# Kernel tuning notes

Hardware: AMD Instinct MI355X
Metric: run time of the kernel (lower is better)

Reference implementation:

```python
import jax, jax.numpy as jnp
import numpy as np

H = 32; L = 4; HEADS = 8; VC = 16; BIG = 1e9

def _unit(v):
    return v * jax.lax.rsqrt(jnp.sum(v * v, -1, keepdims=True) + 1e-8)

def _dihedrals(bb):
    n = bb.shape[0]
    X = bb[:, :3].reshape(n * 3, 3)
    U = _unit(X[1:] - X[:-1])
    u2, u1, u0 = U[:-2], U[1:-1], U[2:]
    n2 = _unit(jnp.cross(u2, u1)); n1 = _unit(jnp.cross(u1, u0))
    cosD = jnp.clip(jnp.sum(n2 * n1, -1), -1 + 1e-6, 1 - 1e-6)
    D = jnp.sign(jnp.sum(u2 * n1, -1)) * jnp.arccos(cosD)
    D = jnp.pad(D, (1, 2)).reshape(n, 3)
    return jnp.concatenate([jnp.cos(D), jnp.sin(D)], -1)

def _orientations(x):
    f = jnp.pad(_unit(x[1:] - x[:-1]), ((0, 1), (0, 0)))
    b = jnp.pad(_unit(x[:-1] - x[1:]), ((1, 0), (0, 0)))
    return jnp.stack([f, b], -2)

def _virtual_cb(bb):
    n_, ca, c = bb[:, 0], bb[:, 1], bb[:, 2]
    b = ca - n_; cc = c - ca; a = jnp.cross(b, cc)
    return -0.58273431 * a + 0.56802827 * b - 0.54067466 * cc + ca

def _rbf(d, nbin=16, dmax=20.0):
    mu = jnp.linspace(0.0, dmax, nbin); sig = dmax / nbin
    return jnp.exp(-(((d[..., None] - mu) / sig) ** 2))

def _pos_emb(didx, nemb=16):
    freq = jnp.exp(jnp.arange(0, nemb, 2, dtype=jnp.float32) * (-np.log(10000.0) / nemb))
    ang = didx[..., None].astype(jnp.float32) * freq
    return jnp.concatenate([jnp.cos(ang), jnp.sin(ang)], -1)

def _edge_rot(vec):
    # per-edge rotation aligning edge direction to e_y (equiformer-style)
    nrm = _unit(vec)
    helper = jnp.where(jnp.abs(nrm[..., 2:3]) > 0.99, jnp.array([1.0, 0.0, 0.0]), jnp.array([0.0, 0.0, 1.0]))
    z = _unit(jnp.cross(nrm, helper))
    x = jnp.cross(nrm, z)
    return jnp.stack([x, nrm, z], axis=-2)

def _rot(R, x):
    return jnp.concatenate([x[..., :1, :], jnp.einsum('...ij,...jc->...ic', R, x[..., 1:, :])], -2)

def _rot_inv(R, x):
    return jnp.concatenate([x[..., :1, :], jnp.einsum('...ji,...jc->...ic', R, x[..., 1:, :])], -2)

def _norm_so3(x, g0, b0, g1):
    x0 = x[..., 0, :]; x1 = x[..., 1:, :]
    mu = jnp.mean(x0, -1, keepdims=True)
    var = jnp.var(x0, -1, keepdims=True)
    y0 = (x0 - mu) * jax.lax.rsqrt(var + 1e-6) * g0 + b0
    y1 = x1 * jax.lax.rsqrt(jnp.mean(x1 * x1, (-2, -1), keepdims=True) + 1e-6) * g1
    return jnp.concatenate([y0[..., None, :], y1], -2)

def _project(xin, nbr, R, ef, rw1, rw2, ow):
    src = _rot(R, xin[nbr])                         # [N,k,4,Cin] gather + rotate into edge frame
    rad = jax.nn.silu(ef @ rw1) @ rw2               # [N,k,Cin] radial weights
    msg = _rot_inv(R, src * rad[..., None, :])      # rotate back to global frame
    return jnp.mean(msg, axis=1) @ ow               # [N,4,Cout]

def _forward(bb, latent, ln_g0, ln_b0, ln_g1, bb_rad_w1, bb_rad_w2, bb_out_w,
             lat_rad_w1, lat_rad_w2, lat_out_w, tln_g0, tln_b0, tln_g1,
             attn_w1, attn_w2, v_w, o_w, ffn_w1, ffn_w2, ffn_wg, ffn_v1,
             eu_w1, eu_w2, out_rad_w1, out_rad_w2, out_w,
             seq_w1, seq_b1, seq_w2, seq_b2, seq_w3, seq_b3, x_mask, n_per, k):
    N = bb.shape[0]
    Xca = bb[:, 1]
    # backbone SO3 features [N,4,7]: l=0 dihedrals (padded to 7), l=1 seven vectors
    dih = jnp.pad(_dihedrals(bb), ((0, 0), (0, 1)))
    vecs = jnp.concatenate([bb - Xca[:, None], _orientations(Xca),
                            (_virtual_cb(bb) - Xca)[:, None]], -2)
    bb_feat = jnp.concatenate([dih[:, None, :], jnp.nan_to_num(jnp.swapaxes(vecs, -1, -2))], 1)
    # kNN graph within each chain; masked residues pushed far away
    batch = jnp.arange(N) // n_per
    mx = jnp.where(x_mask[:, None], BIG, Xca)
    sq = jnp.sum(mx * mx, -1)
    d2 = sq[:, None] + sq[None, :] - 2.0 * (mx @ mx.T)
    bad = (batch[:, None] != batch[None, :]) | jnp.eye(N, dtype=bool)
    d2 = jnp.where(bad, BIG, d2)
    _, nbr = jax.lax.top_k(-d2, k)                  # [N,k] source indices per target
    edge_vec = Xca[:, None] - Xca[nbr]
    R = _edge_rot(edge_vec)                         # [N,k,3,3]
    dist = jnp.sqrt(jnp.sum(edge_vec * edge_vec, -1) + 1e-12)
    ef = jnp.concatenate([_rbf(dist), _pos_emb(nbr - jnp.arange(N)[:, None])], -1)  # [N,k,32]
    lat = _norm_so3(latent, ln_g0, ln_b0, ln_g1)
    x = jnp.concatenate([_project(bb_feat, nbr, R, ef, bb_rad_w1, bb_rad_w2, bb_out_w),
                         _project(lat, nbr, R, ef, lat_rad_w1, lat_rad_w2, lat_out_w)], -1)  # [N,4,H]
    for l in range(L):
        xl = _norm_so3(x, tln_g0[l], tln_b0[l], tln_g1[l])
        src = xl[nbr]                               # [N,k,4,H]
        feat = jnp.concatenate([src[..., 0, :],
                                jnp.broadcast_to(xl[:, None, 0, :], src[..., 0, :].shape),
                                ef], -1)            # [N,k,3H]
        alpha = jax.nn.softmax(jax.nn.silu(feat @ attn_w1[l]) @ attn_w2[l], axis=1)  # [N,k,heads]
        v = _rot_inv(R, _rot(R, src) @ v_w[l])      # [N,k,4,heads*vc]
        v = v.reshape(N, k, 4, HEADS, VC)
        agg = jnp.einsum('nkh,nkchv->nchv', alpha, v).reshape(N, 4, HEADS * VC)
        x = x + agg @ o_w[l]
        h = jax.nn.silu(x[:, 0, :] @ ffn_w1[l])
        gate = jax.nn.sigmoid(h @ ffn_wg[l])
        x = x + jnp.concatenate([(h @ ffn_w2[l])[:, None, :],
                                 (x[:, 1:, :] @ ffn_v1[l]) * gate[:, None, :]], 1)
        e_in = jnp.concatenate([ef, x[nbr][..., 0, :],
                                jnp.broadcast_to(x[:, None, 0, :], (N, k, H))], -1)
        ef = ef + jax.nn.silu(e_in @ eu_w1[l]) @ eu_w2[l]
    atoms = _project(x, nbr, R, ef, out_rad_w1, out_rad_w2, out_w)  # [N,4,91]
    decoded_latent = jnp.swapaxes(atoms[:, 1:4, :], -1, -2)         # [N,91,3]
    hh = jax.nn.relu(x[:, 0, :] @ seq_w1 + seq_b1)
    hh = jax.nn.relu(hh @ seq_w2 + seq_b2)
    seq_logits = jax.nn.log_softmax(hh @ seq_w3 + seq_b3, -1)
    return decoded_latent, seq_logits

def setup_inputs() -> dict:
    key = jax.random.key(0)
    N = 8192; n_per = 2048; k = 30
    keys = iter(jax.random.split(key, 64))
    def W(shape):
        fan = shape[-2] if len(shape) > 1 else shape[-1]
        return (jax.random.normal(next(keys), shape) / np.sqrt(fan)).astype(jnp.float32)
    inp = {
        'bb': (jax.random.normal(next(keys), (N, 4, 3)) * 3.0).astype(jnp.float32),
        'latent': jax.random.normal(next(keys), (N, 4, H), dtype=jnp.float32),
        'ln_g0': jnp.ones((H,), jnp.float32), 'ln_b0': jnp.zeros((H,), jnp.float32), 'ln_g1': jnp.ones((H,), jnp.float32),
        'bb_rad_w1': W((H, 64)), 'bb_rad_w2': W((64, 7)), 'bb_out_w': W((7, 16)),
        'lat_rad_w1': W((H, 64)), 'lat_rad_w2': W((64, H)), 'lat_out_w': W((H, 16)),
        'tln_g0': jnp.ones((L, H), jnp.float32), 'tln_b0': jnp.zeros((L, H), jnp.float32), 'tln_g1': jnp.ones((L, H), jnp.float32),
        'attn_w1': W((L, 3 * H, H)), 'attn_w2': W((L, H, HEADS)),
        'v_w': W((L, H, HEADS * VC)), 'o_w': W((L, HEADS * VC, H)),
        'ffn_w1': W((L, H, 2 * H)), 'ffn_w2': W((L, 2 * H, H)), 'ffn_wg': W((L, 2 * H, H)), 'ffn_v1': W((L, H, H)),
        'eu_w1': W((L, 3 * H, 2 * H)), 'eu_w2': W((L, 2 * H, H)),
        'out_rad_w1': W((H, 64)), 'out_rad_w2': W((64, H)), 'out_w': W((H, 91)),
        'seq_w1': W((H, 64)), 'seq_b1': jnp.zeros((64,), jnp.float32),
        'seq_w2': W((64, H)), 'seq_b2': jnp.zeros((H,), jnp.float32),
        'seq_w3': W((H, 20)), 'seq_b3': jnp.zeros((20,), jnp.float32),
        'x_mask': jnp.zeros((N,), bool), 'n_per': n_per, 'k': k,
    }
    return inp

def reference(bb, latent, ln_g0, ln_b0, ln_g1, bb_rad_w1, bb_rad_w2, bb_out_w,
              lat_rad_w1, lat_rad_w2, lat_out_w, tln_g0, tln_b0, tln_g1,
              attn_w1, attn_w2, v_w, o_w, ffn_w1, ffn_w2, ffn_wg, ffn_v1,
              eu_w1, eu_w2, out_rad_w1, out_rad_w2, out_w,
              seq_w1, seq_b1, seq_w2, seq_b2, seq_w3, seq_b3, x_mask, n_per, k):
    return _forward(bb, latent, ln_g0, ln_b0, ln_g1, bb_rad_w1, bb_rad_w2, bb_out_w,
                    lat_rad_w1, lat_rad_w2, lat_out_w, tln_g0, tln_b0, tln_g1,
                    attn_w1, attn_w2, v_w, o_w, ffn_w1, ffn_w2, ffn_wg, ffn_v1,
                    eu_w1, eu_w2, out_rad_w1, out_rad_w2, out_w,
                    seq_w1, seq_b1, seq_w2, seq_b2, seq_w3, seq_b3, x_mask, n_per, k)
```

## Files before the change

### kernel.cpp

```cpp
#include <hip/hip_runtime.h>
#include <math.h>

#define NRES 8192
#define NPER 2048
#define KNB  30
#define NEDGE (NRES*KNB)

typedef float v2f __attribute__((ext_vector_type(2)));

__device__ __forceinline__ float siluf(float x){ return x / (1.0f + __expf(-x)); }
__device__ __forceinline__ v2f splat2(float a){ v2f r; r.x=a; r.y=a; return r; }

__global__ void k_bbfeat(const float* __restrict__ bb, float* __restrict__ bbf,
                         float4* __restrict__ ca){
  int n = blockIdx.x*256 + threadIdx.x;
  if(n >= NRES) return;
  const float* r = bb + n*12;
  float cax=r[3], cay=r[4], caz=r[5];
  ca[n] = make_float4(cax,cay,caz, cax*cax+cay*cay+caz*caz);
  float vx[7],vy[7],vz[7];
  for(int a=0;a<4;a++){ vx[a]=r[a*3]-cax; vy[a]=r[a*3+1]-cay; vz[a]=r[a*3+2]-caz; }
  if(n<NRES-1){
    float dx=bb[(n+1)*12+3]-cax, dy=bb[(n+1)*12+4]-cay, dz=bb[(n+1)*12+5]-caz;
    float s=rsqrtf(dx*dx+dy*dy+dz*dz+1e-8f);
    vx[4]=dx*s; vy[4]=dy*s; vz[4]=dz*s;
  } else { vx[4]=0.f; vy[4]=0.f; vz[4]=0.f; }
  if(n>0){
    float dx=bb[(n-1)*12+3]-cax, dy=bb[(n-1)*12+4]-cay, dz=bb[(n-1)*12+5]-caz;
    float s=rsqrtf(dx*dx+dy*dy+dz*dz+1e-8f);
    vx[5]=dx*s; vy[5]=dy*s; vz[5]=dz*s;
  } else { vx[5]=0.f; vy[5]=0.f; vz[5]=0.f; }
  {
    float bx=cax-r[0], by=cay-r[1], bz=caz-r[2];
    float cx=r[6]-cax, cy=r[7]-cay, cz=r[8]-caz;
    float axx=by*cz-bz*cy, ayy=bz*cx-bx*cz, azz=bx*cy-by*cx;
    vx[6]=-0.58273431f*axx+0.56802827f*bx-0.54067466f*cx;
    vy[6]=-0.58273431f*ayy+0.56802827f*by-0.54067466f*cy;
    vz[6]=-0.58273431f*azz+0.56802827f*bz-0.54067466f*cz;
  }
  float cD[3], sD[3];
  for(int t=0;t<3;t++){
    cD[t]=1.0f; sD[t]=0.0f;
    int f=3*n+t-1;
    if(f>=0 && f<3*NRES-3){
      float X[4][3];
      for(int q=0;q<4;q++){
        int m=f+q, rr=m/3, aa=m-rr*3;
        X[q][0]=bb[rr*12+aa*3]; X[q][1]=bb[rr*12+aa*3+1]; X[q][2]=bb[rr*12+aa*3+2];
      }
      float u2x=X[1][0]-X[0][0], u2y=X[1][1]-X[0][1], u2z=X[1][2]-X[0][2];
      float u1x=X[2][0]-X[1][0], u1y=X[2][1]-X[1][1], u1z=X[2][2]-X[1][2];
      float u0x=X[3][0]-X[2][0], u0y=X[3][1]-X[2][1], u0z=X[3][2]-X[2][2];
      float s2=rsqrtf(u2x*u2x+u2y*u2y+u2z*u2z+1e-8f); u2x*=s2; u2y*=s2; u2z*=s2;
      float s1=rsqrtf(u1x*u1x+u1y*u1y+u1z*u1z+1e-8f); u1x*=s1; u1y*=s1; u1z*=s1;
      float s0=rsqrtf(u0x*u0x+u0y*u0y+u0z*u0z+1e-8f); u0x*=s0; u0y*=s0; u0z*=s0;
      float n2x=u2y*u1z-u2z*u1y, n2y=u2z*u1x-u2x*u1z, n2z=u2x*u1y-u2y*u1x;
      float nn2=rsqrtf(n2x*n2x+n2y*n2y+n2z*n2z+1e-8f); n2x*=nn2; n2y*=nn2; n2z*=nn2;
      float n1x=u1y*u0z-u1z*u0y, n1y=u1z*u0x-u1x*u0z, n1z=u1x*u0y-u1y*u0x;
      float nn1=rsqrtf(n1x*n1x+n1y*n1y+n1z*n1z+1e-8f); n1x*=nn1; n1y*=nn1; n1z*=nn1;
      float dotn = n2x*n1x+n2y*n1y+n2z*n1z;
      float cosD = fminf(fmaxf(dotn, -1.0f+1e-6f), 1.0f-1e-6f);
      float sg = u2x*n1x+u2y*n1y+u2z*n1z;
      if(sg==0.0f){ cD[t]=1.0f; sD[t]=0.0f; }
      else {
        float sgn = (sg>0.0f)?1.0f:-1.0f;
        cD[t]=cosD;
        sD[t]=sgn*sqrtf(fmaxf(1.0f-cosD*cosD,0.0f));
      }
    }
  }
  float* o = bbf + n*28;
  o[0]=cD[0]; o[1]=cD[1]; o[2]=cD[2]; o[3]=sD[0]; o[4]=sD[1]; o[5]=sD[2]; o[6]=0.f;
  for(int c=0;c<7;c++){ o[7+c]=vx[c]; o[14+c]=vy[c]; o[21+c]=vz[c]; }
}

__device__ __forceinline__ unsigned long long knn_extract(const float* __restrict__ vals,
                                                          unsigned &mask, int lane){
  float bm=INFINITY; int ba=0;
  #pragma unroll
  for(int t=0;t<32;t++){
    if(!((mask>>t)&1u) && vals[t]<bm){ bm=vals[t]; ba=t; }
  }
  mask |= 1u<<ba;
  unsigned ub = __float_as_uint(bm);
  ub ^= (ub & 0x80000000u) ? 0xFFFFFFFFu : 0x80000000u;
  return ((unsigned long long)ub<<32) | (unsigned)(ba*64+lane);
}

__global__ __launch_bounds__(256) void k_knn(const float4* __restrict__ ca, int* __restrict__ nbr){
  __shared__ float sx[NPER], sy[NPER], sz[NPER], sq[NPER];
  int wave = threadIdx.x>>6;
  int lane = threadIdx.x&63;
  int i = blockIdx.x*4 + wave;
  int batch = i / NPER;
  int base = batch*NPER;
  for(int t=threadIdx.x; t<NPER; t+=256){
    float4 c = ca[base+t];
    sx[t]=c.x; sy[t]=c.y; sz[t]=c.z; sq[t]=c.w;
  }
  __syncthreads();
  int il = i - base;
  float xi=sx[il], yi=sy[il], zi=sz[il], si=sq[il];
  float vals[32];
  #pragma unroll
  for(int t=0;t<32;t++){
    int j = t*64 + lane;
    float d2 = si + sq[j] - 2.0f*(xi*sx[j]+yi*sy[j]+zi*sz[j]);
    if(j==il) d2 = 1e30f;
    vals[t]=d2;
  }
  unsigned mask = 0;
  unsigned long long s0 = knn_extract(vals, mask, lane);
  unsigned long long s1 = knn_extract(vals, mask, lane);
  unsigned long long s2 = knn_extract(vals, mask, lane);
  unsigned long long s3 = knn_extract(vals, mask, lane);
  const unsigned long long EMPTY = ~0ull;
  for(int it=0; it<KNB; it++){
    unsigned long long m = s0;
    #pragma unroll
    for(int off=32; off>0; off>>=1){
      unsigned long long o = __shfl_xor(m, off, 64);
      m = (o<m) ? o : m;
    }
    if(lane==0) nbr[i*KNB+it] = base + (int)(m & 0x7FFull);
    if((int)(m & 63ull) == lane){
      s0=s1; s1=s2; s2=s3; s3=EMPTY;
      if(s0==EMPTY) s0 = knn_extract(vals, mask, lane);
    }
  }
}

__global__ void k_tbl(float* __restrict__ tbl){
  int i = blockIdx.x*256 + threadIdx.x;
  int d = i>>3, m = i&7;
  float freq = __expf(-1.1512925465f*(float)m);
  float ang = (float)(d-2048)*freq;
  tbl[d*16+m]   = cosf(ang);
  tbl[d*16+8+m] = sinf(ang);
}

__global__ void k_edgefeat(const float4* __restrict__ ca, const int* __restrict__ nbr,
                           const float* __restrict__ tbl, float* __restrict__ ef){
  int e = blockIdx.x*256 + threadIdx.x;
  if(e >= NEDGE) return;
  int n = e/KNB;
  int j = nbr[e];
  float4 cn = ca[n], cj = ca[j];
  float dx=cn.x-cj.x, dy=cn.y-cj.y, dz=cn.z-cj.z;
  float dist = sqrtf(dx*dx+dy*dy+dz*dz + 1e-12f);
  float f[32];
  #pragma unroll
  for(int m=0;m<16;m++){
    float mu = (20.0f/15.0f)*(float)m;
    float t = (dist-mu)*(1.0f/1.25f);
    f[m] = __expf(-t*t);
  }
  {
    const float4* t4 = (const float4*)(tbl + (size_t)(j - n + 2048)*16);
    float4 c0=t4[0], c1=t4[1], s0=t4[2], s1=t4[3];
    f[16]=c0.x; f[17]=c0.y; f[18]=c0.z; f[19]=c0.w;
    f[20]=c1.x; f[21]=c1.y; f[22]=c1.z; f[23]=c1.w;
    f[24]=s0.x; f[25]=s0.y; f[26]=s0.z; f[27]=s0.w;
    f[28]=s1.x; f[29]=s1.y; f[30]=s1.z; f[31]=s1.w;
  }
  float4* o4 = (float4*)(ef + (size_t)e*32);
  #pragma unroll
  for(int q=0;q<8;q++) o4[q] = make_float4(f[q*4],f[q*4+1],f[q*4+2],f[q*4+3]);
}

__global__ void k_norm(const float* __restrict__ in, float* __restrict__ out,
                       const float* __restrict__ g0, const float* __restrict__ b0,
                       const float* __restrict__ g1){
  int tid = blockIdx.x*256 + threadIdx.x;
  int n = tid >> 5, lane = tid & 31;
  if(n >= NRES) return;
  const float* xn = in + n*128;
  float x0 = xn[lane];
  float s = x0, s2 = x0*x0;
  for(int off=16; off>0; off>>=1){ s += __shfl_xor(s, off, 32); s2 += __shfl_xor(s2, off, 32); }
  float mu = s*(1.0f/32.0f);
  float var = s2*(1.0f/32.0f) - mu*mu;
  float y0 = (x0-mu)*rsqrtf(var+1e-6f)*g0[lane] + b0[lane];
  float v1 = xn[32+lane], v2 = xn[64+lane], v3 = xn[96+lane];
  float ss = v1*v1+v2*v2+v3*v3;
  for(int off=16; off>0; off>>=1){ ss += __shfl_xor(ss, off, 32); }
  float sc = rsqrtf(ss*(1.0f/96.0f) + 1e-6f);
  float g = g1[lane];
  out[n*128+lane]     = y0;
  out[n*128+32+lane]  = v1*sc*g;
  out[n*128+64+lane]  = v2*sc*g;
  out[n*128+96+lane]  = v3*sc*g;
}

__device__ __forceinline__ void load32(float* __restrict__ f, const float* __restrict__ src){
  const float4* s4 = (const float4*)src;
  #pragma unroll
  for(int q=0;q<8;q++){
    float4 v = s4[q];
    f[q*4+0]=v.x; f[q*4+1]=v.y; f[q*4+2]=v.z; f[q*4+3]=v.w;
  }
}

__global__ __launch_bounds__(128, 4)
void k_rad(const float* __restrict__ ef,
           const float* __restrict__ bbw1, const float* __restrict__ bbw2,
           const float* __restrict__ latw1, const float* __restrict__ latw2,
           float* __restrict__ radbb, float* __restrict__ radlat){
  int e = blockIdx.x*128 + threadIdx.x;
  float f[32];
  load32(f, ef + (size_t)e*32);
  float ab[7];
  #pragma unroll
  for(int t=0;t<7;t++) ab[t]=0.f;
  #pragma unroll
  for(int half=0; half<2; half++){
    v2f h[16];
    #pragma unroll
    for(int o=0;o<16;o++) h[o]=splat2(0.f);
    #pragma unroll
    for(int c=0;c<32;c++){
      v2f fc = splat2(f[c]);
      const v2f* w = (const v2f*)(bbw1 + c*64 + half*32);
      #pragma unroll
      for(int o=0;o<16;o++) h[o] += fc*w[o];
    }
    #pragma unroll
    for(int o=0;o<16;o++){
      float v0 = siluf(h[o].x), v1 = siluf(h[o].y);
      const float* wa = bbw2 + (half*32+o*2)*7;
      const float* wb = bbw2 + (half*32+o*2+1)*7;
      #pragma unroll
      for(int t=0;t<7;t++) ab[t] += v0*wa[t];
      #pragma unroll
      for(int t=0;t<7;t++) ab[t] += v1*wb[t];
    }
  }
  {
    float4* rb4 = (float4*)(radbb + (size_t)e*8);
    rb4[0] = make_float4(ab[0],ab[1],ab[2],ab[3]);
    rb4[1] = make_float4(ab[4],ab[5],ab[6],0.f);
  }
  v2f al[16];
  #pragma unroll
  for(int t=0;t<16;t++) al[t]=splat2(0.f);
  #pragma unroll
  for(int half=0; half<2; half++){
    v2f h[16];
    #pragma unroll
    for(int o=0;o<16;o++) h[o]=splat2(0.f);
    #pragma unroll
    for(int c=0;c<32;c++){
      v2f fc = splat2(f[c]);
      const v2f* w = (const v2f*)(latw1 + c*64 + half*32);
      #pragma unroll
      for(int o=0;o<16;o++) h[o] += fc*w[o];
    }
    #pragma unroll
    for(int o=0;o<16;o++){
      float v0 = siluf(h[o].x), v1 = siluf(h[o].y);
      const v2f* wa = (const v2f*)(latw2 + (half*32+o*2)*32);
      const v2f* wb = (const v2f*)(latw2 + (half*32+o*2+1)*32);
      v2f va = splat2(v0), vb = splat2(v1);
      #pragma unroll
      for(int t=0;t<16;t++) al[t] += va*wa[t];
      #pragma unroll
      for(int t=0;t<16;t++) al[t] += vb*wb[t];
    }
  }
  v2f* rl2 = (v2f*)(radlat + (size_t)e*32);
  #pragma unroll
  for(int q=0;q<16;q++) rl2[q] = al[q];
}

__global__ __launch_bounds__(256) void k_init(const int* __restrict__ nbr,
                       const float* __restrict__ radbb, const float* __restrict__ radlat,
                       const float* __restrict__ bbf, const float* __restrict__ latn,
                       const float* __restrict__ bboutw, const float* __restrict__ latoutw,
                       const float* __restrict__ g0, const float* __restrict__ b0,
                       const float* __restrict__ g1,
                       float* __restrict__ x, float* __restrict__ xl){
  __shared__ float msgbb[4][32], msglat[4][128], xout[4][128];
  int g = threadIdx.x>>6, t = threadIdx.x&63;
  int n = blockIdx.x*4 + g;
  int t31 = t&31, t7 = t%7;
  float accL0=0.f, accL1=0.f, accB=0.f;
  for(int kk=0; kk<KNB; kk++){
    int e = n*KNB+kk;
    int j = nbr[e];
    float rl = radlat[(size_t)e*32 + t31];
    accL0 += latn[j*128+t]    * rl;
    accL1 += latn[j*128+64+t] * rl;
    if(t<28) accB += bbf[j*28+t]*radbb[(size_t)e*8 + t7];
  }
  msglat[g][t]=accL0*(1.0f/KNB); msglat[g][64+t]=accL1*(1.0f/KNB);
  if(t<28) msgbb[g][t]=accB*(1.0f/KNB);
  for(int half=0; half<2; half++){
    int e = half*64+t;
    int rrow = e>>5, c = e&31;
    float v=0.f;
    if(c<16){ for(int q=0;q<7;q++)  v += msgbb[g][rrow*7+q]*bboutw[q*16+c]; }
    else    { for(int q=0;q<32;q++) v += msglat[g][rrow*32+q]*latoutw[q*16+(c-16)]; }
    xout[g][e]=v;
    x[n*128+e]=v;
  }
  if(t<32){
    float x0=xout[g][t];
    float s=x0, s2=x0*x0;
    for(int off=16; off>0; off>>=1){ s+=__shfl_xor(s,off,32); s2+=__shfl_xor(s2,off,32); }
    float mu=s*(1.0f/32.0f), var=s2*(1.0f/32.0f)-mu*mu;
    float y0=(x0-mu)*rsqrtf(var+1e-6f)*g0[t]+b0[t];
    float v1=xout[g][32+t], v2=xout[g][64+t], v3=xout[g][96+t];
    float ss=v1*v1+v2*v2+v3*v3;
    for(int off=16; off>0; off>>=1) ss+=__shfl_xor(ss,off,32);
    float sc=rsqrtf(ss*(1.0f/96.0f)+1e-6f);
    float gg=g1[t];
    xl[n*128+t]=y0; xl[n*128+32+t]=v1*sc*gg; xl[n*128+64+t]=v2*sc*gg; xl[n*128+96+t]=v3*sc*gg;
  }
}

__global__ __launch_bounds__(256) void k_nodeprep(const float* __restrict__ x,
                       const float* __restrict__ xl,
                       const float* __restrict__ ew1, const float* __restrict__ aw1,
                       float* __restrict__ hsrc, float* __restrict__ hdst,
                       float* __restrict__ asrc, float* __restrict__ adst){
  __shared__ float sx[4][32], sl[4][32];
  int g = threadIdx.x>>6, lane = threadIdx.x&63;
  int n = blockIdx.x*4 + g;
  if(lane<32){
    if(x)   sx[g][lane] = x[n*128+lane];
    if(aw1) sl[g][lane] = xl[n*128+lane];
  }
  __syncthreads();
  if(x){
    float a0=0.f, a1=0.f;
    #pragma unroll
    for(int c=0;c<32;c++){
      float xv = sx[g][c];
      a0 += xv*ew1[(32+c)*64+lane];
      a1 += xv*ew1[(64+c)*64+lane];
    }
    hsrc[n*64+lane]=a0; hdst[n*64+lane]=a1;
  }
  if(aw1){
    int o = lane&31;
    int roff = (lane>=32)? 32 : 0;
    float a=0.f;
    #pragma unroll
    for(int c=0;c<32;c++) a += sl[g][c]*aw1[(roff+c)*32+o];
    if(lane<32) asrc[n*32+o]=a; else adst[n*32+o]=a;
  }
}

__global__ __launch_bounds__(128, 4)
void k_logits(const int* __restrict__ nbr,
              const float* __restrict__ asrc, const float* __restrict__ adst,
              const float* __restrict__ ef, const float* __restrict__ w1,
              const float* __restrict__ w2, float* __restrict__ logits){
  int e = blockIdx.x*128 + threadIdx.x;
  int n = e/KNB;
  int j = nbr[e];
  v2f h[16];
  {
    const v2f* pj = (const v2f*)(asrc + (size_t)j*32);
    const v2f* pn = (const v2f*)(adst + (size_t)n*32);
    #pragma unroll
    for(int q=0;q<16;q++) h[q] = pj[q]+pn[q];
  }
  float f[32];
  load32(f, ef + (size_t)e*32);
  #pragma unroll
  for(int c=0;c<32;c++){
    v2f fc = splat2(f[c]);
    const v2f* w = (const v2f*)(w1 + (64+c)*32);
    #pragma unroll
    for(int o=0;o<16;o++) h[o] += fc*w[o];
  }
  v2f acc[4];
  #pragma unroll
  for(int t=0;t<4;t++) acc[t]=splat2(0.f);
  #pragma unroll
  for(int o=0;o<16;o++){
    float v0 = siluf(h[o].x), v1 = siluf(h[o].y);
    const v2f* wa = (const v2f*)(w2 + (o*2)*8);
    const v2f* wb = (const v2f*)(w2 + (o*2+1)*8);
    v2f va = splat2(v0), vb = splat2(v1);
    #pragma unroll
    for(int t=0;t<4;t++) acc[t] += va*wa[t];
    #pragma unroll
    for(int t=0;t<4;t++) acc[t] += vb*wb[t];
  }
  v2f* lg2 = (v2f*)(logits + (size_t)e*8);
  #pragma unroll
  for(int q=0;q<4;q++) lg2[q] = acc[q];
}

__global__ __launch_bounds__(256) void k_update(const int* __restrict__ nbr, const float* __restrict__ xl,
                         const float* __restrict__ logits, float* __restrict__ x,
                         float* __restrict__ xlout,
                         const float* __restrict__ vw, const float* __restrict__ ow,
                         const float* __restrict__ fw1, const float* __restrict__ fw2,
                         const float* __restrict__ fwg, const float* __restrict__ fv1,
                         const float* __restrict__ g0, const float* __restrict__ b0,
                         const float* __restrict__ g1){
  __shared__ float S_lg[4][240], S_m[4][8], S_inv[4][8];
  __shared__ float S_S[4][1024], S_agg[4][512], S_x[4][128];
  __shared__ float S_h[4][64], S_g[4][32], S_d0[4][32];
  int g = threadIdx.x>>6, t = threadIdx.x&63;
  int n = blockIdx.x*4 + g;
  for(int r=t; r<240; r+=64) S_lg[g][r] = logits[(size_t)n*240+r];
  if(t<8){
    float m=-1e30f;
    for(int kk=0;kk<KNB;kk++) m=fmaxf(m, S_lg[g][kk*8+t]);
    float s=0.f;
    for(int kk=0;kk<KNB;kk++) s += __expf(S_lg[g][kk*8+t]-m);
    S_m[g][t]=m; S_inv[g][t]=1.0f/s;
  }
  for(int r=t; r<240; r+=64){ int h=r&7; S_lg[g][r]=__expf(S_lg[g][r]-S_m[g][h])*S_inv[g][h]; }
  int hd = t>>3, i8 = t&7;
  const float4* xl4 = (const float4*)xl;
  float acc[16];
  for(int m=0;m<16;m++) acc[m]=0.f;
  for(int kk=0;kk<KNB;kk++){
    int j=nbr[n*KNB+kk];
    float a = S_lg[g][kk*8+hd];
    float4 b0v = xl4[j*32 + i8*4 + 0];
    float4 b1v = xl4[j*32 + i8*4 + 1];
    float4 b2v = xl4[j*32 + i8*4 + 2];
    float4 b3v = xl4[j*32 + i8*4 + 3];
    acc[0]+=a*b0v.x; acc[1]+=a*b0v.y; acc[2]+=a*b0v.z; acc[3]+=a*b0v.w;
    acc[4]+=a*b1v.x; acc[5]+=a*b1v.y; acc[6]+=a*b1v.z; acc[7]+=a*b1v.w;
    acc[8]+=a*b2v.x; acc[9]+=a*b2v.y; acc[10]+=a*b2v.z; acc[11]+=a*b2v.w;
    acc[12]+=a*b3v.x; acc[13]+=a*b3v.y; acc[14]+=a*b3v.z; acc[15]+=a*b3v.w;
  }
  for(int m=0;m<16;m++) S_S[g][hd*128 + i8*16 + m] = acc[m];
  for(int half=0; half<2; half++){
    int hv = half*64+t;
    int hh = hv>>4;
    float a0=0.f,a1=0.f,a2=0.f,a3=0.f;
    for(int c=0;c<32;c++){
      float w = vw[c*128+hv];
      a0 += S_S[g][hh*128 + c]*w;
      a1 += S_S[g][hh*128 + 32+c]*w;
      a2 += S_S[g][hh*128 + 64+c]*w;
      a3 += S_S[g][hh*128 + 96+c]*w;
    }
    S_agg[g][hv]=a0; S_agg[g][128+hv]=a1; S_agg[g][256+hv]=a2; S_agg[g][384+hv]=a3;
  }
  for(int half=0; half<2; half++){
    int e = half*64+t;
    int rrow = e>>5, c = e&31;
    float v = x[n*128+e];
    for(int hv=0;hv<128;hv++) v += S_agg[g][rrow*128+hv]*ow[hv*32+c];
    S_x[g][e]=v;
  }
  {
    float hs=0.f;
    for(int c=0;c<32;c++) hs += S_x[g][c]*fw1[c*64+t];
    S_h[g][t]=siluf(hs);
  }
  if(t<32){
    float gs=0.f, d0=0.f;
    for(int c=0;c<64;c++){ float hv=S_h[g][c]; gs += hv*fwg[c*32+t]; d0 += hv*fw2[c*32+t]; }
    S_g[g][t]=1.0f/(1.0f+__expf(-gs));
    S_d0[g][t]=d0;
  }
  for(int half=0; half<2; half++){
    int e = half*64+t;
    int rrow = e>>5, c = e&31;
    float xv = S_x[g][e], outv;
    if(rrow==0){ outv = xv + S_d0[g][c]; }
    else {
      float dv=0.f;
      for(int cc=0;cc<32;cc++) dv += S_x[g][rrow*32+cc]*fv1[cc*32+c];
      outv = xv + dv*S_g[g][c];
    }
    S_x[g][e]=outv;
    x[n*128+e]=outv;
  }
  if(t<32){
    float x0=S_x[g][t];
    float s=x0, s2=x0*x0;
    for(int off=16; off>0; off>>=1){ s+=__shfl_xor(s,off,32); s2+=__shfl_xor(s2,off,32); }
    float mu=s*(1.0f/32.0f), var=s2*(1.0f/32.0f)-mu*mu;
    float y0=(x0-mu)*rsqrtf(var+1e-6f)*g0[t]+b0[t];
    float v1=S_x[g][32+t], v2=S_x[g][64+t], v3=S_x[g][96+t];
    float ss=v1*v1+v2*v2+v3*v3;
    for(int off=16; off>0; off>>=1) ss+=__shfl_xor(ss,off,32);
    float sc=rsqrtf(ss*(1.0f/96.0f)+1e-6f);
    float gg=g1[t];
    xlout[n*128+t]=y0; xlout[n*128+32+t]=v1*sc*gg;
    xlout[n*128+64+t]=v2*sc*gg; xlout[n*128+96+t]=v3*sc*gg;
  }
}

__global__ __launch_bounds__(128, 4)
void k_efup(const int* __restrict__ nbr,
            const float* __restrict__ hsrc, const float* __restrict__ hdst,
            const float* __restrict__ ew1, const float* __restrict__ ew2,
            float* __restrict__ ef,
            const float* __restrict__ asrc, const float* __restrict__ adst,
            const float* __restrict__ aw1n, const float* __restrict__ aw2n,
            float* __restrict__ logits){
  __shared__ float Sf[128][33];
  int tl = threadIdx.x;
  int e = blockIdx.x*128 + tl;
  int n = e/KNB;
  int j = nbr[e];
  {
    const float4* s4 = (const float4*)(ef + (size_t)e*32);
    #pragma unroll
    for(int q=0;q<8;q++){
      float4 v = s4[q];
      Sf[tl][q*4+0]=v.x; Sf[tl][q*4+1]=v.y; Sf[tl][q*4+2]=v.z; Sf[tl][q*4+3]=v.w;
    }
  }
  v2f acc[16];
  #pragma unroll
  for(int t=0;t<16;t++) acc[t]=splat2(0.f);
  #pragma unroll
  for(int oq=0; oq<4; oq++){
    v2f h[8];
    {
      const float4* pj = (const float4*)(hsrc + (size_t)j*64 + oq*16);
      const float4* pn = (const float4*)(hdst + (size_t)n*64 + oq*16);
      #pragma unroll
      for(int q=0;q<4;q++){
        float4 a=pj[q], b=pn[q];
        h[2*q]   = (v2f){a.x+b.x, a.y+b.y};
        h[2*q+1] = (v2f){a.z+b.z, a.w+b.w};
      }
    }
    #pragma unroll
    for(int c=0;c<32;c++){
      v2f fc = splat2(Sf[tl][c]);
      const v2f* w = (const v2f*)(ew1 + c*64 + oq*16);
      #pragma unroll
      for(int o=0;o<8;o++) h[o] += fc*w[o];
    }
    #pragma unroll
    for(int o=0;o<8;o++){
      float v0 = siluf(h[o].x), v1 = siluf(h[o].y);
      const v2f* wa = (const v2f*)(ew2 + (oq*16+o*2)*32);
      const v2f* wb = (const v2f*)(ew2 + (oq*16+o*2+1)*32);
      v2f va = splat2(v0), vb = splat2(v1);
      #pragma unroll
      for(int t=0;t<16;t++) acc[t] += va*wa[t];
      #pragma unroll
      for(int t=0;t<16;t++) acc[t] += vb*wb[t];
    }
  }
  {
    float4* e4 = (float4*)(ef + (size_t)e*32);
    #pragma unroll
    for(int q=0;q<8;q++){
      float f0 = Sf[tl][q*4+0] + acc[2*q].x;
      float f1 = Sf[tl][q*4+1] + acc[2*q].y;
      float f2 = Sf[tl][q*4+2] + acc[2*q+1].x;
      float f3 = Sf[tl][q*4+3] + acc[2*q+1].y;
      e4[q] = make_float4(f0,f1,f2,f3);
      Sf[tl][q*4+0]=f0; Sf[tl][q*4+1]=f1; Sf[tl][q*4+2]=f2; Sf[tl][q*4+3]=f3;
    }
  }
  v2f h2[16];
  {
    const v2f* pj = (const v2f*)(asrc + (size_t)j*32);
    const v2f* pn = (const v2f*)(adst + (size_t)n*32);
    #pragma unroll
    for(int q=0;q<16;q++) h2[q] = pj[q]+pn[q];
  }
  #pragma unroll
  for(int c=0;c<32;c++){
    v2f fc = splat2(Sf[tl][c]);
    const v2f* w = (const v2f*)(aw1n + (64+c)*32);
    #pragma unroll
    for(int o=0;o<16;o++) h2[o] += fc*w[o];
  }
  v2f a8[4];
  #pragma unroll
  for(int t=0;t<4;t++) a8[t]=splat2(0.f);
  #pragma unroll
  for(int o=0;o<16;o++){
    float v0 = siluf(h2[o].x), v1 = siluf(h2[o].y);
    const v2f* wa = (const v2f*)(aw2n + (o*2)*8);
    const v2f* wb = (const v2f*)(aw2n + (o*2+1)*8);
    v2f va = splat2(v0), vb = splat2(v1);
    #pragma unroll
    for(int t=0;t<4;t++) a8[t] += va*wa[t];
    #pragma unroll
    for(int t=0;t<4;t++) a8[t] += vb*wb[t];
  }
  v2f* lg2 = (v2f*)(logits + (size_t)e*8);
  #pragma unroll
  for(int q=0;q<4;q++) lg2[q] = a8[q];
}

__global__ __launch_bounds__(128, 4)
void k_efup_orad(const int* __restrict__ nbr,
                 const float* __restrict__ hsrc, const float* __restrict__ hdst,
                 const float* __restrict__ ew1, const float* __restrict__ ew2,
                 float* __restrict__ ef,
                 const float* __restrict__ orw1, const float* __restrict__ orw2){
  int e = blockIdx.x*128 + threadIdx.x;
  int n = e/KNB;
  int j = nbr[e];
  float f[32];
  load32(f, ef + (size_t)e*32);
  v2f acc[16];
  #pragma unroll
  for(int t=0;t<16;t++) acc[t]=splat2(0.f);
  #pragma unroll
  for(int half=0; half<2; half++){
    v2f h[16];
    {
      const v2f* pj = (const v2f*)(hsrc + (size_t)j*64 + half*32);
      const v2f* pn = (const v2f*)(hdst + (size_t)n*64 + half*32);
      #pragma unroll
      for(int q=0;q<16;q++) h[q] = pj[q]+pn[q];
    }
    #pragma unroll
    for(int c=0;c<32;c++){
      v2f fc = splat2(f[c]);
      const v2f* w = (const v2f*)(ew1 + c*64 + half*32);
      #pragma unroll
      for(int o=0;o<16;o++) h[o] += fc*w[o];
    }
    #pragma unroll
    for(int o=0;o<16;o++){
      float v0 = siluf(h[o].x), v1 = siluf(h[o].y);
      const v2f* wa = (const v2f*)(ew2 + (half*32+o*2)*32);
      const v2f* wb = (const v2f*)(ew2 + (half*32+o*2+1)*32);
      v2f va = splat2(v0), vb = splat2(v1);
      #pragma unroll
      for(int t=0;t<16;t++) acc[t] += va*wa[t];
      #pragma unroll
      for(int t=0;t<16;t++) acc[t] += vb*wb[t];
    }
  }
  #pragma unroll
  for(int t=0;t<16;t++){ f[2*t] += acc[t].x; f[2*t+1] += acc[t].y; }
  v2f oa[16];
  #pragma unroll
  for(int t=0;t<16;t++) oa[t]=splat2(0.f);
  #pragma unroll
  for(int half=0; half<2; half++){
    v2f h[16];
    #pragma unroll
    for(int o=0;o<16;o++) h[o]=splat2(0.f);
    #pragma unroll
    for(int c=0;c<32;c++){
      v2f fc = splat2(f[c]);
      const v2f* w = (const v2f*)(orw1 + c*64 + half*32);
      #pragma unroll
      for(int o=0;o<16;o++) h[o] += fc*w[o];
    }
    #pragma unroll
    for(int o=0;o<16;o++){
      float v0 = siluf(h[o].x), v1 = siluf(h[o].y);
      const v2f* wa = (const v2f*)(orw2 + (half*32+o*2)*32);
      const v2f* wb = (const v2f*)(orw2 + (half*32+o*2+1)*32);
      v2f va = splat2(v0), vb = splat2(v1);
      #pragma unroll
      for(int t=0;t<16;t++) oa[t] += va*wa[t];
      #pragma unroll
      for(int t=0;t<16;t++) oa[t] += vb*wb[t];
    }
  }
  v2f* r2 = (v2f*)(ef + (size_t)e*32);
  #pragma unroll
  for(int q=0;q<16;q++) r2[q] = oa[q];
}

__global__ __launch_bounds__(256) void k_out(const int* __restrict__ nbr, const float* __restrict__ orad,
                      const float* __restrict__ x,
                      const float* __restrict__ outw,
                      const float* __restrict__ sw1, const float* __restrict__ sb1,
                      const float* __restrict__ sw2, const float* __restrict__ sb2,
                      const float* __restrict__ sw3, const float* __restrict__ sb3,
                      float* __restrict__ out, float* __restrict__ outseq){
  __shared__ float msg[4][128];
  __shared__ float h1[4][64], h2[4][32], lgs[4][20];
  int g = threadIdx.x>>6, t = threadIdx.x&63;
  int n = blockIdx.x*4 + g;
  int t31 = t&31;
  float acc0=0.f, acc1=0.f;
  for(int kk=0;kk<KNB;kk++){
    int e=n*KNB+kk;
    int j=nbr[e];
    float rl = orad[(size_t)e*32 + t31];
    acc0 += x[j*128+t]*rl;
    acc1 += x[j*128+64+t]*rl;
  }
  msg[g][t]=acc0*(1.0f/KNB); msg[g][64+t]=acc1*(1.0f/KNB);
  for(int o=t;o<91;o+=64){
    for(int rrow=1;rrow<4;rrow++){
      float s=0.f;
      for(int c=0;c<32;c++) s += msg[g][rrow*32+c]*outw[c*91+o];
      out[(size_t)n*273 + o*3 + (rrow-1)] = s;
    }
  }
  {
    float s=0.f;
    for(int c=0;c<32;c++) s += x[n*128+c]*sw1[c*64+t];
    h1[g][t]=fmaxf(s+sb1[t],0.f);
  }
  if(t<32){
    float s=0.f;
    for(int c=0;c<64;c++) s += h1[g][c]*sw2[c*32+t];
    h2[g][t]=fmaxf(s+sb2[t],0.f);
  }
  if(t<20){
    float s=0.f;
    for(int c=0;c<32;c++) s += h2[g][c]*sw3[c*20+t];
    lgs[g][t]=s+sb3[t];
  }
  if(t<20){
    float m=-1e30f;
    for(int c=0;c<20;c++) m=fmaxf(m,lgs[g][c]);
    float se=0.f;
    for(int c=0;c<20;c++) se += __expf(lgs[g][c]-m);
    outseq[(size_t)n*20+t]=lgs[g][t]-m-logf(se);
  }
}

extern "C" void kernel_launch(void* const* d_in, const int* in_sizes, int n_in,
                              void* d_out, int out_size, void* d_ws, size_t ws_size,
                              hipStream_t stream) {
  const float* bb      = (const float*)d_in[0];
  const float* latent  = (const float*)d_in[1];
  const float* ln_g0   = (const float*)d_in[2];
  const float* ln_b0   = (const float*)d_in[3];
  const float* ln_g1   = (const float*)d_in[4];
  const float* bbw1    = (const float*)d_in[5];
  const float* bbw2    = (const float*)d_in[6];
  const float* bboutw  = (const float*)d_in[7];
  const float* latw1   = (const float*)d_in[8];
  const float* latw2   = (const float*)d_in[9];
  const float* latoutw = (const float*)d_in[10];
  const float* tg0     = (const float*)d_in[11];
  const float* tb0     = (const float*)d_in[12];
  const float* tg1     = (const float*)d_in[13];
  const float* aw1     = (const float*)d_in[14];
  const float* aw2     = (const float*)d_in[15];
  const float* vw      = (const float*)d_in[16];
  const float* ow      = (const float*)d_in[17];
  const float* fw1     = (const float*)d_in[18];
  const float* fw2     = (const float*)d_in[19];
  const float* fwg     = (const float*)d_in[20];
  const float* fv1     = (const float*)d_in[21];
  const float* ew1     = (const float*)d_in[22];
  const float* ew2     = (const float*)d_in[23];
  const float* orw1    = (const float*)d_in[24];
  const float* orw2    = (const float*)d_in[25];
  const float* outw    = (const float*)d_in[26];
  const float* sw1     = (const float*)d_in[27];
  const float* sb1     = (const float*)d_in[28];
  const float* sw2     = (const float*)d_in[29];
  const float* sb2     = (const float*)d_in[30];
  const float* sw3     = (const float*)d_in[31];
  const float* sb3     = (const float*)d_in[32];
  float* outp = (float*)d_out;

  int*    nbr    = (int*)d_ws;
  float*  ef     = (float*)((char*)d_ws + 1024*1024);
  float*  xbuf   = ef   + (size_t)NEDGE*32;
  float*  xlA    = xbuf + (size_t)NRES*128;
  float*  xlB    = xlA  + (size_t)NRES*128;
  float*  bbf    = xlB  + (size_t)NRES*128;
  float*  logits = bbf  + (size_t)NRES*28;
  float4* ca     = (float4*)(logits + (size_t)NEDGE*8);
  float*  edgescratch = (float*)(ca + NRES);
  float*  radbb  = logits;
  float*  radlat = edgescratch;
  float*  tbl    = xbuf;
  float*  hsrc   = edgescratch;
  float*  hdst   = edgescratch + (size_t)NRES*64;
  float*  asrc   = edgescratch + (size_t)NRES*128;
  float*  adst   = edgescratch + (size_t)NRES*128 + (size_t)NRES*32;

  k_bbfeat  <<<NRES/256, 256, 0, stream>>>(bb, bbf, ca);
  k_knn     <<<NRES/4,   256, 0, stream>>>(ca, nbr);
  k_tbl     <<<4096*8/256, 256, 0, stream>>>(tbl);
  k_edgefeat<<<NEDGE/256, 256, 0, stream>>>(ca, nbr, tbl, ef);
  k_norm    <<<NRES*32/256, 256, 0, stream>>>(latent, xlA, ln_g0, ln_b0, ln_g1);
  k_rad     <<<NEDGE/128, 128, 0, stream>>>(ef, bbw1, bbw2, latw1, latw2, radbb, radlat);
  k_init    <<<NRES/4, 256, 0, stream>>>(nbr, radbb, radlat, bbf, xlA,
                                         bboutw, latoutw,
                                         tg0, tb0, tg1,
                                         xbuf, xlB);
  k_nodeprep<<<NRES/4, 256, 0, stream>>>(nullptr, xlB, ew1, aw1, hsrc, hdst, asrc, adst);
  k_logits  <<<NEDGE/128, 128, 0, stream>>>(nbr, asrc, adst, ef, aw1, aw2, logits);
  for(int l=0;l<4;l++){
    const float* xl_in  = (l&1) ? xlA : xlB;
    float*       xl_out = (l&1) ? xlB : xlA;
    int ln = (l+1<4) ? (l+1) : 3;
    k_update <<<NRES/4, 256, 0, stream>>>(nbr, xl_in, logits, xbuf, xl_out,
                                          vw+l*32*128, ow+l*128*32,
                                          fw1+l*32*64, fw2+l*64*32,
                                          fwg+l*64*32, fv1+l*32*32,
                                          tg0+ln*32, tb0+ln*32, tg1+ln*32);
    if(l<3){
      k_nodeprep<<<NRES/4, 256, 0, stream>>>(xbuf, xl_out, ew1+l*96*64, aw1+(l+1)*96*32,
                                             hsrc, hdst, asrc, adst);
      k_efup<<<NEDGE/128, 128, 0, stream>>>(nbr, hsrc, hdst,
                                            ew1+l*96*64, ew2+l*64*32, ef,
                                            asrc, adst,
                                            aw1+(l+1)*96*32, aw2+(l+1)*32*8, logits);
    } else {
      k_nodeprep<<<NRES/4, 256, 0, stream>>>(xbuf, xl_out, ew1+l*96*64, nullptr,
                                             hsrc, hdst, asrc, adst);
      k_efup_orad<<<NEDGE/128, 128, 0, stream>>>(nbr, hsrc, hdst,
                                                 ew1+l*96*64, ew2+l*64*32, ef,
                                                 orw1, orw2);
    }
  }
  k_out <<<NRES/4, 256, 0, stream>>>(nbr, ef , xbuf, outw,
                                     sw1, sb1, sw2, sb2, sw3, sb3,
                                     outp, outp + (size_t)NRES*273);
}
```

Baseline: 1.140 ms.

## Split each edge's MLP work across two threads with shuffle exchange

The per-edge update kernels k_efup and k_efup_orad now assign two threads to each edge instead of one. Each thread computes half of the hidden units and half of the outputs, and the two threads trade hidden activations with __shfl_xor. Edge features are staged in shared memory, and the launch bound rises to allow more resident blocks. The aim is to cut per-thread register pressure and serial FMA chains so occupancy and latency hiding improve, at the cost of twice as many threads, extra shuffles and duplicated gather loads.

```diff
diff --git a/kernel.cpp b/kernel.cpp
--- a/kernel.cpp
+++ b/kernel.cpp
@@ -493,7 +493,7 @@
   }
 }
 
-__global__ __launch_bounds__(128, 4)
+__global__ __launch_bounds__(128, 6)
 void k_efup(const int* __restrict__ nbr,
             const float* __restrict__ hsrc, const float* __restrict__ hdst,
             const float* __restrict__ ew1, const float* __restrict__ ew2,
@@ -501,173 +501,231 @@
             const float* __restrict__ asrc, const float* __restrict__ adst,
             const float* __restrict__ aw1n, const float* __restrict__ aw2n,
             float* __restrict__ logits){
-  __shared__ float Sf[128][33];
-  int tl = threadIdx.x;
-  int e = blockIdx.x*128 + tl;
+  __shared__ float Sf[64][33];
+  int tid = threadIdx.x;
+  int le = tid>>1, p = tid&1;
+  int e = blockIdx.x*64 + le;
   int n = e/KNB;
   int j = nbr[e];
   {
     const float4* s4 = (const float4*)(ef + (size_t)e*32);
     #pragma unroll
+    for(int q=0;q<4;q++){
+      float4 v = s4[p*4+q];
+      int b = (p*4+q)*4;
+      Sf[le][b+0]=v.x; Sf[le][b+1]=v.y; Sf[le][b+2]=v.z; Sf[le][b+3]=v.w;
+    }
+  }
+  float s[32];
+  {
+    v2f h[16];
+    const float4* pj = (const float4*)(hsrc + (size_t)j*64 + p*32);
+    const float4* pn = (const float4*)(hdst + (size_t)n*64 + p*32);
+    #pragma unroll
     for(int q=0;q<8;q++){
-      float4 v = s4[q];
-      Sf[tl][q*4+0]=v.x; Sf[tl][q*4+1]=v.y; Sf[tl][q*4+2]=v.z; Sf[tl][q*4+3]=v.w;
-    }
-  }
-  v2f acc[16];
-  #pragma unroll
-  for(int t=0;t<16;t++) acc[t]=splat2(0.f);
-  #pragma unroll
-  for(int oq=0; oq<4; oq++){
-    v2f h[8];
-    {
-      const float4* pj = (const float4*)(hsrc + (size_t)j*64 + oq*16);
-      const float4* pn = (const float4*)(hdst + (size_t)n*64 + oq*16);
-      #pragma unroll
-      for(int q=0;q<4;q++){
-        float4 a=pj[q], b=pn[q];
-        h[2*q]   = (v2f){a.x+b.x, a.y+b.y};
-        h[2*q+1] = (v2f){a.z+b.z, a.w+b.w};
-      }
+      float4 a=pj[q], b=pn[q];
+      h[2*q]   = (v2f){a.x+b.x, a.y+b.y};
+      h[2*q+1] = (v2f){a.z+b.z, a.w+b.w};
     }
     #pragma unroll
     for(int c=0;c<32;c++){
-      v2f fc = splat2(Sf[tl][c]);
-      const v2f* w = (const v2f*)(ew1 + c*64 + oq*16);
-      #pragma unroll
-      for(int o=0;o<8;o++) h[o] += fc*w[o];
-    }
-    #pragma unroll
-    for(int o=0;o<8;o++){
-      float v0 = siluf(h[o].x), v1 = siluf(h[o].y);
-      const v2f* wa = (const v2f*)(ew2 + (oq*16+o*2)*32);
-      const v2f* wb = (const v2f*)(ew2 + (oq*16+o*2+1)*32);
-      v2f va = splat2(v0), vb = splat2(v1);
-      #pragma unroll
-      for(int t=0;t<16;t++) acc[t] += va*wa[t];
-      #pragma unroll
-      for(int t=0;t<16;t++) acc[t] += vb*wb[t];
-    }
-  }
-  {
+      v2f fc = splat2(Sf[le][c]);
+      const v2f* w = (const v2f*)(ew1 + c*64 + p*32);
+      #pragma unroll
+      for(int o=0;o<16;o++) h[o] += fc*w[o];
+    }
+    #pragma unroll
+    for(int o=0;o<16;o++){ s[2*o]=siluf(h[o].x); s[2*o+1]=siluf(h[o].y); }
+  }
+  v2f acc[8];
+  #pragma unroll
+  for(int t=0;t<8;t++) acc[t]=splat2(0.f);
+  #pragma unroll
+  for(int i=0;i<32;i++){
+    float r = __shfl_xor(s[i], 1, 64);
+    float v = p ? r : s[i];
+    const v2f* w = (const v2f*)(ew2 + i*32 + p*16);
+    v2f vv = splat2(v);
+    #pragma unroll
+    for(int t=0;t<8;t++) acc[t] += vv*w[t];
+  }
+  #pragma unroll
+  for(int i=0;i<32;i++){
+    float r = __shfl_xor(s[i], 1, 64);
+    float v = p ? s[i] : r;
+    const v2f* w = (const v2f*)(ew2 + (32+i)*32 + p*16);
+    v2f vv = splat2(v);
+    #pragma unroll
+    for(int t=0;t<8;t++) acc[t] += vv*w[t];
+  }
+  {
+    float nf[16];
+    #pragma unroll
+    for(int t=0;t<8;t++){
+      nf[2*t]   = Sf[le][p*16+2*t]   + acc[t].x;
+      nf[2*t+1] = Sf[le][p*16+2*t+1] + acc[t].y;
+    }
     float4* e4 = (float4*)(ef + (size_t)e*32);
     #pragma unroll
-    for(int q=0;q<8;q++){
-      float f0 = Sf[tl][q*4+0] + acc[2*q].x;
-      float f1 = Sf[tl][q*4+1] + acc[2*q].y;
-      float f2 = Sf[tl][q*4+2] + acc[2*q+1].x;
-      float f3 = Sf[tl][q*4+3] + acc[2*q+1].y;
-      e4[q] = make_float4(f0,f1,f2,f3);
-      Sf[tl][q*4+0]=f0; Sf[tl][q*4+1]=f1; Sf[tl][q*4+2]=f2; Sf[tl][q*4+3]=f3;
-    }
-  }
-  v2f h2[16];
-  {
-    const v2f* pj = (const v2f*)(asrc + (size_t)j*32);
-    const v2f* pn = (const v2f*)(adst + (size_t)n*32);
-    #pragma unroll
-    for(int q=0;q<16;q++) h2[q] = pj[q]+pn[q];
-  }
-  #pragma unroll
-  for(int c=0;c<32;c++){
-    v2f fc = splat2(Sf[tl][c]);
-    const v2f* w = (const v2f*)(aw1n + (64+c)*32);
-    #pragma unroll
-    for(int o=0;o<16;o++) h2[o] += fc*w[o];
-  }
-  v2f a8[4];
-  #pragma unroll
-  for(int t=0;t<4;t++) a8[t]=splat2(0.f);
-  #pragma unroll
-  for(int o=0;o<16;o++){
-    float v0 = siluf(h2[o].x), v1 = siluf(h2[o].y);
-    const v2f* wa = (const v2f*)(aw2n + (o*2)*8);
-    const v2f* wb = (const v2f*)(aw2n + (o*2+1)*8);
-    v2f va = splat2(v0), vb = splat2(v1);
-    #pragma unroll
-    for(int t=0;t<4;t++) a8[t] += va*wa[t];
-    #pragma unroll
-    for(int t=0;t<4;t++) a8[t] += vb*wb[t];
-  }
-  v2f* lg2 = (v2f*)(logits + (size_t)e*8);
-  #pragma unroll
-  for(int q=0;q<4;q++) lg2[q] = a8[q];
-}
-
-__global__ __launch_bounds__(128, 4)
+    for(int q=0;q<4;q++)
+      e4[p*4+q] = make_float4(nf[q*4],nf[q*4+1],nf[q*4+2],nf[q*4+3]);
+    #pragma unroll
+    for(int i=0;i<16;i++) Sf[le][p*16+i] = nf[i];
+  }
+  float s2v[16];
+  {
+    v2f h2[8];
+    const float4* pj = (const float4*)(asrc + (size_t)j*32 + p*16);
+    const float4* pn = (const float4*)(adst + (size_t)n*32 + p*16);
+    #pragma unroll
+    for(int q=0;q<4;q++){
+      float4 a=pj[q], b=pn[q];
+      h2[2*q]   = (v2f){a.x+b.x, a.y+b.y};
+      h2[2*q+1] = (v2f){a.z+b.z, a.w+b.w};
+    }
+    #pragma unroll
+    for(int c=0;c<32;c++){
+      v2f fc = splat2(Sf[le][c]);
+      const v2f* w = (const v2f*)(aw1n + (64+c)*32 + p*16);
+      #pragma unroll
+      for(int o=0;o<8;o++) h2[o] += fc*w[o];
+    }
+    #pragma unroll
+    for(int o=0;o<8;o++){ s2v[2*o]=siluf(h2[o].x); s2v[2*o+1]=siluf(h2[o].y); }
+  }
+  v2f a8[2];
+  a8[0]=splat2(0.f); a8[1]=splat2(0.f);
+  #pragma unroll
+  for(int i=0;i<16;i++){
+    float r = __shfl_xor(s2v[i], 1, 64);
+    float v = p ? r : s2v[i];
+    const v2f* w = (const v2f*)(aw2n + i*8 + p*4);
+    v2f vv = splat2(v);
+    a8[0] += vv*w[0]; a8[1] += vv*w[1];
+  }
+  #pragma unroll
+  for(int i=0;i<16;i++){
+    float r = __shfl_xor(s2v[i], 1, 64);
+    float v = p ? s2v[i] : r;
+    const v2f* w = (const v2f*)(aw2n + (16+i)*8 + p*4);
+    v2f vv = splat2(v);
+    a8[0] += vv*w[0]; a8[1] += vv*w[1];
+  }
+  *(float4*)(logits + (size_t)e*8 + p*4) = make_float4(a8[0].x,a8[0].y,a8[1].x,a8[1].y);
+}
+
+__global__ __launch_bounds__(128, 6)
 void k_efup_orad(const int* __restrict__ nbr,
                  const float* __restrict__ hsrc, const float* __restrict__ hdst,
                  const float* __restrict__ ew1, const float* __restrict__ ew2,
                  float* __restrict__ ef,
                  const float* __restrict__ orw1, const float* __restrict__ orw2){
-  int e = blockIdx.x*128 + threadIdx.x;
+  __shared__ float Sf[64][33];
+  int tid = threadIdx.x;
+  int le = tid>>1, p = tid&1;
+  int e = blockIdx.x*64 + le;
   int n = e/KNB;
   int j = nbr[e];
-  float f[32];
-  load32(f, ef + (size_t)e*32);
-  v2f acc[16];
-  #pragma unroll
-  for(int t=0;t<16;t++) acc[t]=splat2(0.f);
-  #pragma unroll
-  for(int half=0; half<2; half++){
+  {
+    const float4* s4 = (const float4*)(ef + (size_t)e*32);
+    #pragma unroll
+    for(int q=0;q<4;q++){
+      float4 v = s4[p*4+q];
+      int b = (p*4+q)*4;
+      Sf[le][b+0]=v.x; Sf[le][b+1]=v.y; Sf[le][b+2]=v.z; Sf[le][b+3]=v.w;
+    }
+  }
+  float s[32];
+  {
     v2f h[16];
-    {
-      const v2f* pj = (const v2f*)(hsrc + (size_t)j*64 + half*32);
-      const v2f* pn = (const v2f*)(hdst + (size_t)n*64 + half*32);
-      #pragma unroll
-      for(int q=0;q<16;q++) h[q] = pj[q]+pn[q];
+    const float4* pj = (const float4*)(hsrc + (size_t)j*64 + p*32);
+    const float4* pn = (const float4*)(hdst + (size_t)n*64 + p*32);
+    #pragma unroll
+    for(int q=0;q<8;q++){
+      float4 a=pj[q], b=pn[q];
+      h[2*q]   = (v2f){a.x+b.x, a.y+b.y};
+      h[2*q+1] = (v2f){a.z+b.z, a.w+b.w};
     }
     #pragma unroll
     for(int c=0;c<32;c++){
-      v2f fc = splat2(f[c]);
-      const v2f* w = (const v2f*)(ew1 + c*64 + half*32);
+      v2f fc = splat2(Sf[le][c]);
+      const v2f* w = (const v2f*)(ew1 + c*64 + p*32);
       #pragma unroll
       for(int o=0;o<16;o++) h[o] += fc*w[o];
     }
     #pragma unroll
-    for(int o=0;o<16;o++){
-      float v0 = siluf(h[o].x), v1 = siluf(h[o].y);
-      const v2f* wa = (const v2f*)(ew2 + (half*32+o*2)*32);
-      const v2f* wb = (const v2f*)(ew2 + (half*32+o*2+1)*32);
-      v2f va = splat2(v0), vb = splat2(v1);
-      #pragma unroll
-      for(int t=0;t<16;t++) acc[t] += va*wa[t];
-      #pragma unroll
-      for(int t=0;t<16;t++) acc[t] += vb*wb[t];
-    }
-  }
-  #pragma unroll
-  for(int t=0;t<16;t++){ f[2*t] += acc[t].x; f[2*t+1] += acc[t].y; }
-  v2f oa[16];
-  #pragma unroll
-  for(int t=0;t<16;t++) oa[t]=splat2(0.f);
-  #pragma unroll
-  for(int half=0; half<2; half++){
+    for(int o=0;o<16;o++){ s[2*o]=siluf(h[o].x); s[2*o+1]=siluf(h[o].y); }
+  }
+  v2f acc[8];
+  #pragma unroll
+  for(int t=0;t<8;t++) acc[t]=splat2(0.f);
+  #pragma unroll
+  for(int i=0;i<32;i++){
+    float r = __shfl_xor(s[i], 1, 64);
+    float v = p ? r : s[i];
+    const v2f* w = (const v2f*)(ew2 + i*32 + p*16);
+    v2f vv = splat2(v);
+    #pragma unroll
+    for(int t=0;t<8;t++) acc[t] += vv*w[t];
+  }
+  #pragma unroll
+  for(int i=0;i<32;i++){
+    float r = __shfl_xor(s[i], 1, 64);
+    float v = p ? s[i] : r;
+    const v2f* w = (const v2f*)(ew2 + (32+i)*32 + p*16);
+    v2f vv = splat2(v);
+    #pragma unroll
+    for(int t=0;t<8;t++) acc[t] += vv*w[t];
+  }
+  #pragma unroll
+  for(int t=0;t<8;t++){
+    Sf[le][p*16+2*t]   += acc[t].x;
+    Sf[le][p*16+2*t+1] += acc[t].y;
+  }
+  float s3[32];
+  {
     v2f h[16];
     #pragma unroll
     for(int o=0;o<16;o++) h[o]=splat2(0.f);
     #pragma unroll
     for(int c=0;c<32;c++){
-      v2f fc = splat2(f[c]);
-      const v2f* w = (const v2f*)(orw1 + c*64 + half*32);
+      v2f fc = splat2(Sf[le][c]);
+      const v2f* w = (const v2f*)(orw1 + c*64 + p*32);
       #pragma unroll
       for(int o=0;o<16;o++) h[o] += fc*w[o];
     }
     #pragma unroll
-    for(int o=0;o<16;o++){
-      float v0 = siluf(h[o].x), v1 = siluf(h[o].y);
-      const v2f* wa = (const v2f*)(orw2 + (half*32+o*2)*32);
-      const v2f* wb = (const v2f*)(orw2 + (half*32+o*2+1)*32);
-      v2f va = splat2(v0), vb = splat2(v1);
-      #pragma unroll
-      for(int t=0;t<16;t++) oa[t] += va*wa[t];
-      #pragma unroll
-      for(int t=0;t<16;t++) oa[t] += vb*wb[t];
-    }
-  }
-  v2f* r2 = (v2f*)(ef + (size_t)e*32);
-  #pragma unroll
-  for(int q=0;q<16;q++) r2[q] = oa[q];
+    for(int o=0;o<16;o++){ s3[2*o]=siluf(h[o].x); s3[2*o+1]=siluf(h[o].y); }
+  }
+  v2f oa[8];
+  #pragma unroll
+  for(int t=0;t<8;t++) oa[t]=splat2(0.f);
+  #pragma unroll
+  for(int i=0;i<32;i++){
+    float r = __shfl_xor(s3[i], 1, 64);
+    float v = p ? r : s3[i];
+    const v2f* w = (const v2f*)(orw2 + i*32 + p*16);
+    v2f vv = splat2(v);
+    #pragma unroll
+    for(int t=0;t<8;t++) oa[t] += vv*w[t];
+  }
+  #pragma unroll
+  for(int i=0;i<32;i++){
+    float r = __shfl_xor(s3[i], 1, 64);
+    float v = p ? s3[i] : r;
+    const v2f* w = (const v2f*)(orw2 + (32+i)*32 + p*16);
+    v2f vv = splat2(v);
+    #pragma unroll
+    for(int t=0;t<8;t++) oa[t] += vv*w[t];
+  }
+  {
+    float4* r4 = (float4*)(ef + (size_t)e*32);
+    #pragma unroll
+    for(int q=0;q<2;q++){
+      r4[p*4+q*2]   = make_float4(oa[q*4].x,  oa[q*4].y,  oa[q*4+1].x, oa[q*4+1].y);
+      r4[p*4+q*2+1] = make_float4(oa[q*4+2].x,oa[q*4+2].y,oa[q*4+3].x, oa[q*4+3].y);
+    }
+  }
 }
 
 __global__ __launch_bounds__(256) void k_out(const int* __restrict__ nbr, const float* __restrict__ orad,
@@ -801,16 +859,16 @@
     if(l<3){
       k_nodeprep<<<NRES/4, 256, 0, stream>>>(xbuf, xl_out, ew1+l*96*64, aw1+(l+1)*96*32,
                                              hsrc, hdst, asrc, adst);
-      k_efup<<<NEDGE/128, 128, 0, stream>>>(nbr, hsrc, hdst,
-                                            ew1+l*96*64, ew2+l*64*32, ef,
-                                            asrc, adst,
-                                            aw1+(l+1)*96*32, aw2+(l+1)*32*8, logits);
+      k_efup<<<NEDGE/64, 128, 0, stream>>>(nbr, hsrc, hdst,
+                                           ew1+l*96*64, ew2+l*64*32, ef,
+                                           asrc, adst,
+                                           aw1+(l+1)*96*32, aw2+(l+1)*32*8, logits);
     } else {
       k_nodeprep<<<NRES/4, 256, 0, stream>>>(xbuf, xl_out, ew1+l*96*64, nullptr,
                                              hsrc, hdst, asrc, adst);
-      k_efup_orad<<<NEDGE/128, 128, 0, stream>>>(nbr, hsrc, hdst,
-                                                 ew1+l*96*64, ew2+l*64*32, ef,
-                                                 orw1, orw2);
+      k_efup_orad<<<NEDGE/64, 128, 0, stream>>>(nbr, hsrc, hdst,
+                                                ew1+l*96*64, ew2+l*64*32, ef,
+                                                orw1, orw2);
     }
   }
   k_out <<<NRES/4, 256, 0, stream>>>(nbr, ef , xbuf, outw,
```

Measured after the change: 1.922 ms. 68.6% more time.
